# Kernel tuning notes

Measured on AMD Instinct MI355X. Metric: run time of the kernel, lower is better.

## Reference

```python
import jax, jax.numpy as jnp
import numpy as np

N = 20000
E = 320000
IN_FEAT = 256
HID = 256
OUT_FEAT = 128


def setup_inputs() -> dict:
    key = jax.random.key(0)
    ks = jax.random.split(key, 10)
    inp = {
        "x": jax.random.normal(ks[0], (N, IN_FEAT), dtype=jnp.float32),
        "edge_src": jax.random.randint(ks[1], (E,), 0, N, dtype=jnp.int32),
        "edge_dst": jax.random.randint(ks[2], (E,), 0, N, dtype=jnp.int32),
        "edge_w": jax.random.uniform(ks[3], (E,), dtype=jnp.float32),
        # params (Linear weights stored as [out, in], torch convention)
        "W_emb": jax.random.normal(ks[4], (HID, IN_FEAT), dtype=jnp.float32) / np.sqrt(IN_FEAT),
        "W_gc1": jax.random.normal(ks[5], (HID, 2 * HID), dtype=jnp.float32) / np.sqrt(2 * HID),
        "b_gc1": jnp.zeros((HID,), dtype=jnp.float32),
        "W_gc2": jax.random.normal(ks[6], (HID, 2 * HID), dtype=jnp.float32) / np.sqrt(2 * HID),
        "b_gc2": jnp.zeros((HID,), dtype=jnp.float32),
        "W_fc": jax.random.normal(ks[7], (OUT_FEAT, HID), dtype=jnp.float32) / np.sqrt(HID),
    }
    return inp


def reference(x, edge_src, edge_dst, edge_w, W_emb, W_gc1, b_gc1, W_gc2, b_gc2, W_fc):
    n = x.shape[0]

    def adj_mul(h):
        msgs = h[edge_src] * edge_w[:, None]           # [E, hid]
        return jax.ops.segment_sum(msgs, edge_dst, num_segments=n)

    def gconv(h, W, b):
        cat = jnp.concatenate([h, adj_mul(h)], axis=1)  # [N, 2*hid]
        return cat @ W.T + b

    h = x @ W_emb.T                                    # embedding (no bias)
    h = h + jax.nn.relu(gconv(h, W_gc1, b_gc1))        # residual (dropout = eval identity)
    h = h + jax.nn.relu(gconv(h, W_gc2, b_gc2))
    out = h @ W_fc.T                                   # fc_last (no bias)
    out = out / jnp.sqrt(jnp.sum(out * out, axis=1, keepdims=True))
    return out
```

## Files before the change

kernel.cpp:

```cpp
#include <hip/hip_runtime.h>
#include <math.h>

#define N_NODES 20000
#define E_EDGES 320000
#define HID 256
#define OUT_FEAT 128
#define MPAD 20224
#define CAP 64

#define BK 64
#define LSTR 72
#define ISTR 80
#define TSTR 264

typedef __attribute__((ext_vector_type(8))) __bf16 bf16x8;
typedef __attribute__((ext_vector_type(4))) float floatx4;
typedef __attribute__((ext_vector_type(4))) int intx4;

__device__ __forceinline__ void write_int8_shadow(
    const __bf16 (*tile)[TSTR], int row0, int tid,
    unsigned char* __restrict__ h8, float* __restrict__ scl) {
    const int row = tid >> 3;
    const int seg = tid & 7;
    float vals[32];
    float mx = 0.f;
#pragma unroll
    for (int j = 0; j < 32; j++) {
        float v = (float)tile[row][seg * 32 + j];
        vals[j] = v;
        mx = fmaxf(mx, fabsf(v));
    }
#pragma unroll
    for (int m = 1; m <= 4; m <<= 1) mx = fmaxf(mx, __shfl_xor(mx, m));
    const float enc = mx > 0.f ? 127.f / mx : 0.f;
    unsigned int pk[8];
#pragma unroll
    for (int g = 0; g < 8; g++) {
        unsigned int wd = 0;
#pragma unroll
        for (int j = 0; j < 4; j++) {
            int q = (int)rintf(vals[g * 4 + j] * enc);
            q = q > 127 ? 127 : (q < -127 ? -127 : q);
            wd |= ((unsigned int)(q & 0xff)) << (8 * j);
        }
        pk[g] = wd;
    }
    unsigned char* dstp = h8 + (size_t)(row0 + row) * HID + seg * 32;
    *(int4*)dstp        = make_int4(pk[0], pk[1], pk[2], pk[3]);
    *(int4*)(dstp + 16) = make_int4(pk[4], pk[5], pk[6], pk[7]);
    if (seg == 0) scl[row0 + row] = mx * (1.f / 127.f);
}


#define EMB_BLK 316
#define SCAT_BLK 625
#define CONVL_BLK 40
#define CONVR_BLK 64

__global__ __launch_bounds__(512) void front_kernel(
    const float* __restrict__ x, const float* __restrict__ wembf,
    __bf16* __restrict__ hb0, unsigned char* __restrict__ h8, float* __restrict__ scl,
    const int* __restrict__ src, const int* __restrict__ dst,
    const float* __restrict__ w, int* __restrict__ counts, int2* __restrict__ edges,
    const float* __restrict__ w1f, const float* __restrict__ w2f, const float* __restrict__ wfcf,
    __bf16* __restrict__ w1l, __bf16* __restrict__ w2l, __bf16* __restrict__ wfcb,
    unsigned char* __restrict__ w1r8, unsigned char* __restrict__ w2r8,
    float* __restrict__ w1rs, float* __restrict__ w2rs)
{
    __shared__ char smem[64 * 144 + 256 * 144];
    const int bid = blockIdx.x;
    const int tid = threadIdx.x;

    if (bid < EMB_BLK) {
        __bf16* As = (__bf16*)smem;
        __bf16* Bs = (__bf16*)(smem + 64 * 144);
        const int row0 = bid * 64;
        const int wv = tid >> 6, l = tid & 63, lr = l & 15, lq = l >> 4;
        const int wm = wv & 1, wn4 = wv >> 1;

        floatx4 acc[2][4];
#pragma unroll
        for (int i = 0; i < 2; i++)
#pragma unroll
            for (int j = 0; j < 4; j++) acc[i][j] = (floatx4){0.f, 0.f, 0.f, 0.f};

        const int srow = tid >> 3;
        const int skq = (tid & 7) * 8;

        for (int kc = 0; kc < 256; kc += BK) {
            {
                int grow = row0 + srow;
                float4 v0 = make_float4(0.f, 0.f, 0.f, 0.f), v1 = v0;
                if (grow < N_NODES) {
                    const float* xp = x + (size_t)grow * HID + kc + skq;
                    v0 = *(const float4*)xp;
                    v1 = *(const float4*)(xp + 4);
                }
                bf16x8 o;
                o[0] = (__bf16)v0.x; o[1] = (__bf16)v0.y; o[2] = (__bf16)v0.z; o[3] = (__bf16)v0.w;
                o[4] = (__bf16)v1.x; o[5] = (__bf16)v1.y; o[6] = (__bf16)v1.z; o[7] = (__bf16)v1.w;
                *(bf16x8*)&As[srow * LSTR + skq] = o;
            }
#pragma unroll
            for (int r = 0; r < 4; r++) {
                int row = r * 64 + srow;
                const float* wp = wembf + (size_t)row * 256 + kc + skq;
                float4 v0 = *(const float4*)wp;
                float4 v1 = *(const float4*)(wp + 4);
                bf16x8 o;
                o[0] = (__bf16)v0.x; o[1] = (__bf16)v0.y; o[2] = (__bf16)v0.z; o[3] = (__bf16)v0.w;
                o[4] = (__bf16)v1.x; o[5] = (__bf16)v1.y; o[6] = (__bf16)v1.z; o[7] = (__bf16)v1.w;
                *(bf16x8*)&Bs[row * LSTR + skq] = o;
            }
            __syncthreads();
#pragma unroll
            for (int s = 0; s < 2; s++) {
                bf16x8 af[2], bfr[4];
#pragma unroll
                for (int mt = 0; mt < 2; mt++)
                    af[mt] = *(const bf16x8*)&As[(wm * 32 + mt * 16 + lr) * LSTR + s * 32 + lq * 8];
#pragma unroll
                for (int nt = 0; nt < 4; nt++)
                    bfr[nt] = *(const bf16x8*)&Bs[(wn4 * 64 + nt * 16 + lr) * LSTR + s * 32 + lq * 8];
#pragma unroll
                for (int mt = 0; mt < 2; mt++)
#pragma unroll
                    for (int nt = 0; nt < 4; nt++)
                        acc[mt][nt] = __builtin_amdgcn_mfma_f32_16x16x32_bf16(af[mt], bfr[nt], acc[mt][nt], 0, 0, 0);
            }
            __syncthreads();
        }
        __bf16 (*tile)[TSTR] = (__bf16(*)[TSTR])smem;
#pragma unroll
        for (int nt = 0; nt < 4; nt++) {
            const int col = wn4 * 64 + nt * 16 + lr;
#pragma unroll
            for (int mt = 0; mt < 2; mt++) {
                const int lrow = wm * 32 + mt * 16 + lq * 4;
#pragma unroll
                for (int r = 0; r < 4; r++) {
                    float v = acc[mt][nt][r];
                    hb0[(size_t)(row0 + lrow + r) * HID + col] = (__bf16)v;
                    tile[lrow + r][col] = (__bf16)v;
                }
            }
        }
        __syncthreads();
        write_int8_shadow(tile, row0, tid, h8, scl);
    } else if (bid < EMB_BLK + SCAT_BLK) {
        int e = (bid - EMB_BLK) * 512 + tid;
        int d = dst[e];
        int p = atomicAdd(&counts[d], 1);
        edges[(size_t)d * CAP + p] = make_int2(src[e], __float_as_int(w[e]));
    } else if (bid < EMB_BLK + SCAT_BLK + CONVL_BLK) {
        const size_t gi = ((size_t)(bid - EMB_BLK - SCAT_BLK) * 512 + tid) * 8;
        const float* sp; __bf16* dp;
        if (gi < 65536) {
            size_t row = gi >> 8, k = gi & 255;
            sp = w1f + row * 512 + k; dp = w1l + gi;
        } else if (gi < 131072) {
            size_t off = gi - 65536, row = off >> 8, k = off & 255;
            sp = w2f + row * 512 + k; dp = w2l + off;
        } else {
            size_t off = gi - 131072;
            sp = wfcf + off; dp = wfcb + off;
        }
        float4 v0 = *(const float4*)sp;
        float4 v1 = *(const float4*)(sp + 4);
        bf16x8 o;
        o[0] = (__bf16)v0.x; o[1] = (__bf16)v0.y; o[2] = (__bf16)v0.z; o[3] = (__bf16)v0.w;
        o[4] = (__bf16)v1.x; o[5] = (__bf16)v1.y; o[6] = (__bf16)v1.z; o[7] = (__bf16)v1.w;
        *(bf16x8*)dp = o;
    } else {
        const int gw = (bid - EMB_BLK - SCAT_BLK - CONVL_BLK) * 8 + (tid >> 6);
        const int lane = tid & 63;
        const float* Wsrc = (gw < 256) ? w1f : w2f;
        unsigned char* d8 = (gw < 256) ? w1r8 : w2r8;
        float* ds = (gw < 256) ? w1rs : w2rs;
        const int r = gw & 255;
        float4 v = *(const float4*)(Wsrc + (size_t)r * 512 + 256 + lane * 4);
        float mx = fmaxf(fmaxf(fabsf(v.x), fabsf(v.y)), fmaxf(fabsf(v.z), fabsf(v.w)));
#pragma unroll
        for (int m = 1; m <= 32; m <<= 1) mx = fmaxf(mx, __shfl_xor(mx, m));
        const float enc = mx > 0.f ? 127.f / mx : 0.f;
        unsigned int wd = 0;
        float vv[4] = {v.x, v.y, v.z, v.w};
#pragma unroll
        for (int j = 0; j < 4; j++) {
            int q = (int)rintf(vv[j] * enc);
            q = q > 127 ? 127 : (q < -127 ? -127 : q);
            wd |= ((unsigned int)(q & 0xff)) << (8 * j);
        }
        *(unsigned int*)(d8 + (size_t)r * 256 + lane * 4) = wd;
        if (lane == 0) ds[r] = mx * (1.f / 127.f);
    }
}


#define GBM 32
#define AGG_BYTES (4 * GBM * ISTR)
#define ASCL_OFF  AGG_BYTES
#define GEMM_OFF  (AGG_BYTES + 128)
#define TILE_BYTES (GBM * TSTR * 2)

template <bool LAST>
__global__ __launch_bounds__(256, 3) void gconv_kernel(
    const __bf16* __restrict__ hp,
    const unsigned char* __restrict__ h8in, const float* __restrict__ sclin,
    const int* __restrict__ counts, const int2* __restrict__ edges,
    const __bf16* __restrict__ Wl,
    const unsigned char* __restrict__ Wr8, const float* __restrict__ Wrs,
    const float* __restrict__ bias,
    __bf16* __restrict__ hn, unsigned char* __restrict__ h8out, float* __restrict__ sclout,
    const __bf16* __restrict__ Wfc, float* __restrict__ outp)
{
    __shared__ char smem[GEMM_OFF + TILE_BYTES];
    char* As8 = smem;
    float* asclL = (float*)(smem + ASCL_OFF);
    const int tid = threadIdx.x;
    const int row0 = blockIdx.x * GBM;
    const int wv = tid >> 6, l = tid & 63, lr = l & 15, lq = l >> 4;

    {
        const int hw = tid >> 5;
        const int lh = tid & 31;
#pragma unroll 1
        for (int t = 0; t < 4; ++t) {
            const int j = hw * 4 + t;
            const int d = row0 + j;
            const size_t base = (size_t)d * CAP;
            const int cnt = counts[d];
            const int iters = (cnt + 15) >> 4;
            float acc[8];
#pragma unroll
            for (int q = 0; q < 8; q++) acc[q] = 0.f;

            for (int it = 0; it < iters; ++it) {
                const int jb = it * 16;
                const int2* ep = edges + base + jb;
                int4 eh[8];
#pragma unroll
                for (int u = 0; u < 8; u++) eh[u] = *(const int4*)(ep + u * 2);
                int sidx[16]; float ew[16];
#pragma unroll
                for (int u = 0; u < 8; u++) {
                    const bool m0 = (jb + u * 2)     < cnt;
                    const bool m1 = (jb + u * 2 + 1) < cnt;
                    sidx[u * 2]     = m0 ? eh[u].x : 0;
                    ew[u * 2]       = m0 ? __int_as_float(eh[u].y) : 0.f;
                    sidx[u * 2 + 1] = m1 ? eh[u].z : 0;
                    ew[u * 2 + 1]   = m1 ? __int_as_float(eh[u].w) : 0.f;
                }
                float ws[16];
#pragma unroll
                for (int u = 0; u < 16; u++) ws[u] = ew[u] * sclin[sidx[u]];
                uint2 hv[16];
#pragma unroll
                for (int u = 0; u < 16; u++)
                    hv[u] = *(const uint2*)(h8in + (size_t)sidx[u] * HID + lh * 8);
#pragma unroll
                for (int u = 0; u < 16; u++) {
                    const unsigned int a = hv[u].x, b = hv[u].y;
                    const float wu = ws[u];
                    acc[0] = fmaf(wu, (float)(int)(signed char)(a),       acc[0]);
                    acc[1] = fmaf(wu, (float)(int)(signed char)(a >> 8),  acc[1]);
                    acc[2] = fmaf(wu, (float)(int)(signed char)(a >> 16), acc[2]);
                    acc[3] = fmaf(wu, (float)(int)(signed char)(a >> 24), acc[3]);
                    acc[4] = fmaf(wu, (float)(int)(signed char)(b),       acc[4]);
                    acc[5] = fmaf(wu, (float)(int)(signed char)(b >> 8),  acc[5]);
                    acc[6] = fmaf(wu, (float)(int)(signed char)(b >> 16), acc[6]);
                    acc[7] = fmaf(wu, (float)(int)(signed char)(b >> 24), acc[7]);
                }
            }
            float mx = 0.f;
#pragma unroll
            for (int q = 0; q < 8; q++) mx = fmaxf(mx, fabsf(acc[q]));
#pragma unroll
            for (int m = 1; m <= 16; m <<= 1) mx = fmaxf(mx, __shfl_xor(mx, m));
            const float enc = mx > 0.f ? 127.f / mx : 0.f;
            unsigned int w0 = 0, w1v = 0;
#pragma unroll
            for (int jj = 0; jj < 4; jj++) {
                int q0 = (int)rintf(acc[jj] * enc);
                q0 = q0 > 127 ? 127 : (q0 < -127 ? -127 : q0);
                w0 |= ((unsigned int)(q0 & 0xff)) << (8 * jj);
                int q1 = (int)rintf(acc[4 + jj] * enc);
                q1 = q1 > 127 ? 127 : (q1 < -127 ? -127 : q1);
                w1v |= ((unsigned int)(q1 & 0xff)) << (8 * jj);
            }
            *(uint2*)&As8[(((lh >> 3) * GBM) + j) * ISTR + (lh & 7) * 8] = make_uint2(w0, w1v);
            if (lh == 0) asclL[j] = mx * (1.f / 127.f);
        }
    }

    floatx4 acc[2][4];
    intx4 acc8[2][4];
#pragma unroll
    for (int i = 0; i < 2; i++)
#pragma unroll
        for (int j = 0; j < 4; j++) {
            acc[i][j] = (floatx4){0.f, 0.f, 0.f, 0.f};
            acc8[i][j] = (intx4){0, 0, 0, 0};
        }

#pragma unroll
    for (int kc = 0; kc < 256; kc += BK) {
#pragma unroll
        for (int s = 0; s < 2; s++) {
            const int k0 = kc + s * 32 + lq * 8;
            bf16x8 af[2], bfr[4];
#pragma unroll
            for (int mt = 0; mt < 2; mt++)
                af[mt] = *(const bf16x8*)(hp + (size_t)(row0 + mt * 16 + lr) * HID + k0);
#pragma unroll
            for (int nt = 0; nt < 4; nt++)
                bfr[nt] = *(const bf16x8*)(Wl + (size_t)(wv * 64 + nt * 16 + lr) * 256 + k0);
#pragma unroll
            for (int mt = 0; mt < 2; mt++)
#pragma unroll
                for (int nt = 0; nt < 4; nt++)
                    acc[mt][nt] = __builtin_amdgcn_mfma_f32_16x16x32_bf16(af[mt], bfr[nt], acc[mt][nt], 0, 0, 0);
        }
    }

    __syncthreads();

#pragma unroll
    for (int kc = 0; kc < 256; kc += BK) {
        intx4 a8[2], b8[4];
#pragma unroll
        for (int mt = 0; mt < 2; mt++)
            a8[mt] = *(const intx4*)&As8[(((kc >> 6) * GBM) + mt * 16 + lr) * ISTR + lq * 16];
#pragma unroll
        for (int nt = 0; nt < 4; nt++)
            b8[nt] = *(const intx4*)(Wr8 + (size_t)(wv * 64 + nt * 16 + lr) * 256 + kc + lq * 16);
#pragma unroll
        for (int mt = 0; mt < 2; mt++)
#pragma unroll
            for (int nt = 0; nt < 4; nt++)
                acc8[mt][nt] = __builtin_amdgcn_mfma_i32_16x16x64_i8(a8[mt], b8[nt], acc8[mt][nt], 0, 0, 0);
    }

    __bf16 (*tile)[TSTR] = (__bf16(*)[TSTR])(smem + GEMM_OFF);
#pragma unroll
    for (int nt = 0; nt < 4; nt++) {
        const int col = wv * 64 + nt * 16 + lr;
        const float b = bias[col];
        const float wrc = Wrs[col];
#pragma unroll
        for (int mt = 0; mt < 2; mt++) {
            const int lrow = mt * 16 + lq * 4;
#pragma unroll
            for (int r = 0; r < 4; r++) {
                const int row = row0 + lrow + r;
                float gem = acc[mt][nt][r] + (float)acc8[mt][nt][r] * (asclL[lrow + r] * wrc);
                float res = (float)hp[(size_t)row * HID + col];
                float v = res + fmaxf(gem + b, 0.f);
                if (!LAST) hn[(size_t)row * HID + col] = (__bf16)v;
                tile[lrow + r][col] = (__bf16)v;
            }
        }
    }
    __syncthreads();

    if (!LAST) {
        write_int8_shadow(tile, row0, tid, h8out, sclout);
    } else if (wv < 2) {
        floatx4 facc[8];
#pragma unroll
        for (int j = 0; j < 8; j++) facc[j] = (floatx4){0.f, 0.f, 0.f, 0.f};
#pragma unroll
        for (int kt = 0; kt < 256; kt += 32) {
            bf16x8 a = *(const bf16x8*)&tile[wv * 16 + lr][kt + lq * 8];
            bf16x8 bf8[8];
#pragma unroll
            for (int nt = 0; nt < 8; nt++)
                bf8[nt] = *(const bf16x8*)(Wfc + (size_t)(nt * 16 + lr) * 256 + kt + lq * 8);
#pragma unroll
            for (int nt = 0; nt < 8; nt++)
                facc[nt] = __builtin_amdgcn_mfma_f32_16x16x32_bf16(a, bf8[nt], facc[nt], 0, 0, 0);
        }
        float s[4];
#pragma unroll
        for (int r = 0; r < 4; r++) {
            float t = 0.f;
#pragma unroll
            for (int nt = 0; nt < 8; nt++) t = fmaf(facc[nt][r], facc[nt][r], t);
            s[r] = t;
        }
#pragma unroll
        for (int mask = 1; mask <= 8; mask <<= 1) {
#pragma unroll
            for (int r = 0; r < 4; r++) s[r] += __shfl_xor(s[r], mask);
        }
        float inv[4];
#pragma unroll
        for (int r = 0; r < 4; r++) inv[r] = rsqrtf(s[r]);
#pragma unroll
        for (int r = 0; r < 4; r++) {
            int row = row0 + wv * 16 + lq * 4 + r;
            if (row >= N_NODES) continue;
#pragma unroll
            for (int nt = 0; nt < 8; nt++)
                outp[(size_t)row * OUT_FEAT + nt * 16 + lr] = facc[nt][r] * inv[r];
        }
    }
}


extern "C" void kernel_launch(void* const* d_in, const int* in_sizes, int n_in,
                              void* d_out, int out_size, void* d_ws, size_t ws_size,
                              hipStream_t stream) {
    const float* x        = (const float*)d_in[0];
    const int*   edge_src = (const int*)d_in[1];
    const int*   edge_dst = (const int*)d_in[2];
    const float* edge_w   = (const float*)d_in[3];
    const float* W_emb    = (const float*)d_in[4];
    const float* W_gc1    = (const float*)d_in[5];
    const float* b_gc1    = (const float*)d_in[6];
    const float* W_gc2    = (const float*)d_in[7];
    const float* b_gc2    = (const float*)d_in[8];
    const float* W_fc     = (const float*)d_in[9];
    float* out = (float*)d_out;

    char* p = (char*)d_ws;
    const size_t HROW = (size_t)MPAD * HID;
    __bf16* hb0   = (__bf16*)p;             p += HROW * 2;
    __bf16* hb1   = (__bf16*)p;             p += HROW * 2;
    unsigned char* h8a = (unsigned char*)p; p += HROW;
    float*  scla  = (float*)p;              p += (size_t)MPAD * 4;
    unsigned char* h8b = (unsigned char*)p; p += HROW;
    float*  sclb  = (float*)p;              p += (size_t)MPAD * 4;
    __bf16* w1l   = (__bf16*)p;             p += 65536 * 2;
    __bf16* w2l   = (__bf16*)p;             p += 65536 * 2;
    __bf16* wfcb  = (__bf16*)p;             p += 32768 * 2;
    unsigned char* w1r8 = (unsigned char*)p; p += 65536;
    unsigned char* w2r8 = (unsigned char*)p; p += 65536;
    float*  w1rs  = (float*)p;              p += 256 * 4;
    float*  w2rs  = (float*)p;              p += 256 * 4;
    int2*   edges = (int2*)p;               p += (size_t)N_NODES * CAP * 8;
    int*    counts = (int*)p;               p += (size_t)MPAD * 4;

    hipMemsetAsync(counts, 0, (size_t)MPAD * 4, stream);

    front_kernel<<<EMB_BLK + SCAT_BLK + CONVL_BLK + CONVR_BLK, 512, 0, stream>>>(
        x, W_emb, hb0, h8a, scla, edge_src, edge_dst, edge_w, counts, edges,
        W_gc1, W_gc2, W_fc, w1l, w2l, wfcb, w1r8, w2r8, w1rs, w2rs);

    gconv_kernel<false><<<MPAD / GBM, 256, 0, stream>>>(
        hb0, h8a, scla, counts, edges, w1l, w1r8, w1rs, b_gc1,
        hb1, h8b, sclb, nullptr, nullptr);

    gconv_kernel<true><<<MPAD / GBM, 256, 0, stream>>>(
        hb1, h8b, sclb, counts, edges, w2l, w2r8, w2rs, b_gc2,
        nullptr, nullptr, nullptr, wfcb, out);
}
```

Before: 207.6 us.

## Halve gconv row tile and aggregate two rows per wavefront with full-wave lanes

Cuts the gconv block tile from 32 to 16 rows, so the grid has twice as many blocks, and raises the occupancy hint to 4 blocks per CU. Aggregation now maps a full 64-lane wave over the 256-wide feature row (4 bytes per lane) and processes two destination rows at once with interleaved loads, instead of half-waves doing 8 bytes each over 4 rows sequentially. The MFMA GEMMs and epilogue are reduced to a single 16-row M tile, and the int8 shadow writer gains a 16-row variant. Each block now reloads the full weight matrices for half as many rows, which adds weight traffic per output row. Pairing rows also means each pair iterates up to the larger of the two edge counts.

```diff
diff --git a/kernel.cpp b/kernel.cpp
--- a/kernel.cpp
+++ b/kernel.cpp
@@ -17,7 +17,7 @@
 typedef __attribute__((ext_vector_type(4))) float floatx4;
 typedef __attribute__((ext_vector_type(4))) int intx4;
 
-__device__ __forceinline__ void write_int8_shadow(
+__device__ __forceinline__ void write_int8_shadow64(
     const __bf16 (*tile)[TSTR], int row0, int tid,
     unsigned char* __restrict__ h8, float* __restrict__ scl) {
     const int row = tid >> 3;
@@ -48,6 +48,39 @@
     unsigned char* dstp = h8 + (size_t)(row0 + row) * HID + seg * 32;
     *(int4*)dstp        = make_int4(pk[0], pk[1], pk[2], pk[3]);
     *(int4*)(dstp + 16) = make_int4(pk[4], pk[5], pk[6], pk[7]);
+    if (seg == 0) scl[row0 + row] = mx * (1.f / 127.f);
+}
+
+__device__ __forceinline__ void write_int8_shadow16(
+    const __bf16 (*tile)[TSTR], int row0, int tid,
+    unsigned char* __restrict__ h8, float* __restrict__ scl) {
+    const int row = tid >> 4;
+    const int seg = tid & 15;
+    float vals[16];
+    float mx = 0.f;
+#pragma unroll
+    for (int j = 0; j < 16; j++) {
+        float v = (float)tile[row][seg * 16 + j];
+        vals[j] = v;
+        mx = fmaxf(mx, fabsf(v));
+    }
+#pragma unroll
+    for (int m = 1; m <= 8; m <<= 1) mx = fmaxf(mx, __shfl_xor(mx, m));
+    const float enc = mx > 0.f ? 127.f / mx : 0.f;
+    unsigned int pk[4];
+#pragma unroll
+    for (int g = 0; g < 4; g++) {
+        unsigned int wd = 0;
+#pragma unroll
+        for (int j = 0; j < 4; j++) {
+            int q = (int)rintf(vals[g * 4 + j] * enc);
+            q = q > 127 ? 127 : (q < -127 ? -127 : q);
+            wd |= ((unsigned int)(q & 0xff)) << (8 * j);
+        }
+        pk[g] = wd;
+    }
+    unsigned char* dstp = h8 + (size_t)(row0 + row) * HID + seg * 16;
+    *(int4*)dstp = make_int4(pk[0], pk[1], pk[2], pk[3]);
     if (seg == 0) scl[row0 + row] = mx * (1.f / 127.f);
 }
 
@@ -146,7 +179,7 @@
             }
         }
         __syncthreads();
-        write_int8_shadow(tile, row0, tid, h8, scl);
+        write_int8_shadow64(tile, row0, tid, h8, scl);
     } else if (bid < EMB_BLK + SCAT_BLK) {
         int e = (bid - EMB_BLK) * 512 + tid;
         int d = dst[e];
@@ -197,14 +230,14 @@
 }
 
 
-#define GBM 32
+#define GBM 16
 #define AGG_BYTES (4 * GBM * ISTR)
 #define ASCL_OFF  AGG_BYTES
 #define GEMM_OFF  (AGG_BYTES + 128)
 #define TILE_BYTES (GBM * TSTR * 2)
 
 template <bool LAST>
-__global__ __launch_bounds__(256, 3) void gconv_kernel(
+__global__ __launch_bounds__(256, 4) void gconv_kernel(
     const __bf16* __restrict__ hp,
     const unsigned char* __restrict__ h8in, const float* __restrict__ sclin,
     const int* __restrict__ counts, const int2* __restrict__ edges,
@@ -222,104 +255,124 @@
     const int wv = tid >> 6, l = tid & 63, lr = l & 15, lq = l >> 4;
 
     {
-        const int hw = tid >> 5;
-        const int lh = tid & 31;
+        const int w4 = wv * 4;
+        int cnts[4];
+#pragma unroll
+        for (int k = 0; k < 4; k++) cnts[k] = counts[row0 + w4 + k];
 #pragma unroll 1
-        for (int t = 0; t < 4; ++t) {
-            const int j = hw * 4 + t;
-            const int d = row0 + j;
-            const size_t base = (size_t)d * CAP;
-            const int cnt = counts[d];
-            const int iters = (cnt + 15) >> 4;
-            float acc[8];
-#pragma unroll
-            for (int q = 0; q < 8; q++) acc[q] = 0.f;
-
-            for (int it = 0; it < iters; ++it) {
+        for (int pp = 0; pp < 2; ++pp) {
+            const int jA = w4 + pp * 2, jB = jA + 1;
+            const int cntA = cnts[pp * 2], cntB = cnts[pp * 2 + 1];
+            const int cm = cntA > cntB ? cntA : cntB;
+            const int itm = (cm + 15) >> 4;
+            const int2* epA = edges + (size_t)(row0 + jA) * CAP;
+            const int2* epB = edges + (size_t)(row0 + jB) * CAP;
+            float accA[4] = {0.f, 0.f, 0.f, 0.f};
+            float accB[4] = {0.f, 0.f, 0.f, 0.f};
+#pragma unroll 1
+            for (int it = 0; it < itm; ++it) {
                 const int jb = it * 16;
-                const int2* ep = edges + base + jb;
-                int4 eh[8];
-#pragma unroll
-                for (int u = 0; u < 8; u++) eh[u] = *(const int4*)(ep + u * 2);
-                int sidx[16]; float ew[16];
+                int4 ehA[8], ehB[8];
+#pragma unroll
+                for (int u = 0; u < 8; u++) ehA[u] = *(const int4*)(epA + jb + u * 2);
+#pragma unroll
+                for (int u = 0; u < 8; u++) ehB[u] = *(const int4*)(epB + jb + u * 2);
+                float wsA[16]; unsigned int hA[16];
 #pragma unroll
                 for (int u = 0; u < 8; u++) {
-                    const bool m0 = (jb + u * 2)     < cnt;
-                    const bool m1 = (jb + u * 2 + 1) < cnt;
-                    sidx[u * 2]     = m0 ? eh[u].x : 0;
-                    ew[u * 2]       = m0 ? __int_as_float(eh[u].y) : 0.f;
-                    sidx[u * 2 + 1] = m1 ? eh[u].z : 0;
-                    ew[u * 2 + 1]   = m1 ? __int_as_float(eh[u].w) : 0.f;
+                    const bool m0 = (jb + u * 2)     < cntA;
+                    const bool m1 = (jb + u * 2 + 1) < cntA;
+                    const int s0 = m0 ? ehA[u].x : 0;
+                    const int s1 = m1 ? ehA[u].z : 0;
+                    const float w0 = m0 ? __int_as_float(ehA[u].y) : 0.f;
+                    const float w1 = m1 ? __int_as_float(ehA[u].w) : 0.f;
+                    wsA[u * 2]     = w0 * sclin[s0];
+                    wsA[u * 2 + 1] = w1 * sclin[s1];
+                    hA[u * 2]     = *(const unsigned int*)(h8in + (size_t)s0 * HID + l * 4);
+                    hA[u * 2 + 1] = *(const unsigned int*)(h8in + (size_t)s1 * HID + l * 4);
                 }
-                float ws[16];
-#pragma unroll
-                for (int u = 0; u < 16; u++) ws[u] = ew[u] * sclin[sidx[u]];
-                uint2 hv[16];
-#pragma unroll
-                for (int u = 0; u < 16; u++)
-                    hv[u] = *(const uint2*)(h8in + (size_t)sidx[u] * HID + lh * 8);
+                float wsB[16]; unsigned int hB[16];
+#pragma unroll
+                for (int u = 0; u < 8; u++) {
+                    const bool m0 = (jb + u * 2)     < cntB;
+                    const bool m1 = (jb + u * 2 + 1) < cntB;
+                    const int s0 = m0 ? ehB[u].x : 0;
+                    const int s1 = m1 ? ehB[u].z : 0;
+                    const float w0 = m0 ? __int_as_float(ehB[u].y) : 0.f;
+                    const float w1 = m1 ? __int_as_float(ehB[u].w) : 0.f;
+                    wsB[u * 2]     = w0 * sclin[s0];
+                    wsB[u * 2 + 1] = w1 * sclin[s1];
+                    hB[u * 2]     = *(const unsigned int*)(h8in + (size_t)s0 * HID + l * 4);
+                    hB[u * 2 + 1] = *(const unsigned int*)(h8in + (size_t)s1 * HID + l * 4);
+                }
 #pragma unroll
                 for (int u = 0; u < 16; u++) {
-                    const unsigned int a = hv[u].x, b = hv[u].y;
-                    const float wu = ws[u];
-                    acc[0] = fmaf(wu, (float)(int)(signed char)(a),       acc[0]);
-                    acc[1] = fmaf(wu, (float)(int)(signed char)(a >> 8),  acc[1]);
-                    acc[2] = fmaf(wu, (float)(int)(signed char)(a >> 16), acc[2]);
-                    acc[3] = fmaf(wu, (float)(int)(signed char)(a >> 24), acc[3]);
-                    acc[4] = fmaf(wu, (float)(int)(signed char)(b),       acc[4]);
-                    acc[5] = fmaf(wu, (float)(int)(signed char)(b >> 8),  acc[5]);
-                    acc[6] = fmaf(wu, (float)(int)(signed char)(b >> 16), acc[6]);
-                    acc[7] = fmaf(wu, (float)(int)(signed char)(b >> 24), acc[7]);
+                    const unsigned int a = hA[u];
+                    const float w = wsA[u];
+                    accA[0] = fmaf(w, (float)(int)(signed char)(a),       accA[0]);
+                    accA[1] = fmaf(w, (float)(int)(signed char)(a >> 8),  accA[1]);
+                    accA[2] = fmaf(w, (float)(int)(signed char)(a >> 16), accA[2]);
+                    accA[3] = fmaf(w, (float)(int)(signed char)(a >> 24), accA[3]);
                 }
-            }
-            float mx = 0.f;
-#pragma unroll
-            for (int q = 0; q < 8; q++) mx = fmaxf(mx, fabsf(acc[q]));
-#pragma unroll
-            for (int m = 1; m <= 16; m <<= 1) mx = fmaxf(mx, __shfl_xor(mx, m));
-            const float enc = mx > 0.f ? 127.f / mx : 0.f;
-            unsigned int w0 = 0, w1v = 0;
-#pragma unroll
-            for (int jj = 0; jj < 4; jj++) {
-                int q0 = (int)rintf(acc[jj] * enc);
-                q0 = q0 > 127 ? 127 : (q0 < -127 ? -127 : q0);
-                w0 |= ((unsigned int)(q0 & 0xff)) << (8 * jj);
-                int q1 = (int)rintf(acc[4 + jj] * enc);
-                q1 = q1 > 127 ? 127 : (q1 < -127 ? -127 : q1);
-                w1v |= ((unsigned int)(q1 & 0xff)) << (8 * jj);
-            }
-            *(uint2*)&As8[(((lh >> 3) * GBM) + j) * ISTR + (lh & 7) * 8] = make_uint2(w0, w1v);
-            if (lh == 0) asclL[j] = mx * (1.f / 127.f);
-        }
-    }
-
-    floatx4 acc[2][4];
-    intx4 acc8[2][4];
-#pragma unroll
-    for (int i = 0; i < 2; i++)
-#pragma unroll
-        for (int j = 0; j < 4; j++) {
-            acc[i][j] = (floatx4){0.f, 0.f, 0.f, 0.f};
-            acc8[i][j] = (intx4){0, 0, 0, 0};
-        }
+#pragma unroll
+                for (int u = 0; u < 16; u++) {
+                    const unsigned int a = hB[u];
+                    const float w = wsB[u];
+                    accB[0] = fmaf(w, (float)(int)(signed char)(a),       accB[0]);
+                    accB[1] = fmaf(w, (float)(int)(signed char)(a >> 8),  accB[1]);
+                    accB[2] = fmaf(w, (float)(int)(signed char)(a >> 16), accB[2]);
+                    accB[3] = fmaf(w, (float)(int)(signed char)(a >> 24), accB[3]);
+                }
+            }
+            float mA = fmaxf(fmaxf(fabsf(accA[0]), fabsf(accA[1])), fmaxf(fabsf(accA[2]), fabsf(accA[3])));
+            float mB = fmaxf(fmaxf(fabsf(accB[0]), fabsf(accB[1])), fmaxf(fabsf(accB[2]), fabsf(accB[3])));
+#pragma unroll
+            for (int m = 1; m <= 32; m <<= 1) {
+                mA = fmaxf(mA, __shfl_xor(mA, m));
+                mB = fmaxf(mB, __shfl_xor(mB, m));
+            }
+            const float encA = mA > 0.f ? 127.f / mA : 0.f;
+            const float encB = mB > 0.f ? 127.f / mB : 0.f;
+            unsigned int wdA = 0, wdB = 0;
+#pragma unroll
+            for (int j = 0; j < 4; j++) {
+                int qa = (int)rintf(accA[j] * encA);
+                qa = qa > 127 ? 127 : (qa < -127 ? -127 : qa);
+                wdA |= ((unsigned int)(qa & 0xff)) << (8 * j);
+                int qb = (int)rintf(accB[j] * encB);
+                qb = qb > 127 ? 127 : (qb < -127 ? -127 : qb);
+                wdB |= ((unsigned int)(qb & 0xff)) << (8 * j);
+            }
+            *(unsigned int*)&As8[(((l >> 4) * GBM) + jA) * ISTR + (l & 15) * 4] = wdA;
+            *(unsigned int*)&As8[(((l >> 4) * GBM) + jB) * ISTR + (l & 15) * 4] = wdB;
+            if (l == 0) {
+                asclL[jA] = mA * (1.f / 127.f);
+                asclL[jB] = mB * (1.f / 127.f);
+            }
+        }
+    }
+
+    floatx4 acc[4];
+    intx4 acc8[4];
+#pragma unroll
+    for (int j = 0; j < 4; j++) {
+        acc[j] = (floatx4){0.f, 0.f, 0.f, 0.f};
+        acc8[j] = (intx4){0, 0, 0, 0};
+    }
 
 #pragma unroll
     for (int kc = 0; kc < 256; kc += BK) {
 #pragma unroll
         for (int s = 0; s < 2; s++) {
             const int k0 = kc + s * 32 + lq * 8;
-            bf16x8 af[2], bfr[4];
-#pragma unroll
-            for (int mt = 0; mt < 2; mt++)
-                af[mt] = *(const bf16x8*)(hp + (size_t)(row0 + mt * 16 + lr) * HID + k0);
+            bf16x8 af = *(const bf16x8*)(hp + (size_t)(row0 + lr) * HID + k0);
+            bf16x8 bfr[4];
 #pragma unroll
             for (int nt = 0; nt < 4; nt++)
                 bfr[nt] = *(const bf16x8*)(Wl + (size_t)(wv * 64 + nt * 16 + lr) * 256 + k0);
 #pragma unroll
-            for (int mt = 0; mt < 2; mt++)
-#pragma unroll
-                for (int nt = 0; nt < 4; nt++)
-                    acc[mt][nt] = __builtin_amdgcn_mfma_f32_16x16x32_bf16(af[mt], bfr[nt], acc[mt][nt], 0, 0, 0);
+            for (int nt = 0; nt < 4; nt++)
+                acc[nt] = __builtin_amdgcn_mfma_f32_16x16x32_bf16(af, bfr[nt], acc[nt], 0, 0, 0);
         }
     }
 
@@ -327,18 +380,14 @@
 
 #pragma unroll
     for (int kc = 0; kc < 256; kc += BK) {
-        intx4 a8[2], b8[4];
-#pragma unroll
-        for (int mt = 0; mt < 2; mt++)
-            a8[mt] = *(const intx4*)&As8[(((kc >> 6) * GBM) + mt * 16 + lr) * ISTR + lq * 16];
+        intx4 a8 = *(const intx4*)&As8[(((kc >> 6) * GBM) + lr) * ISTR + lq * 16];
+        intx4 b8[4];
 #pragma unroll
         for (int nt = 0; nt < 4; nt++)
             b8[nt] = *(const intx4*)(Wr8 + (size_t)(wv * 64 + nt * 16 + lr) * 256 + kc + lq * 16);
 #pragma unroll
-        for (int mt = 0; mt < 2; mt++)
-#pragma unroll
-            for (int nt = 0; nt < 4; nt++)
-                acc8[mt][nt] = __builtin_amdgcn_mfma_i32_16x16x64_i8(a8[mt], b8[nt], acc8[mt][nt], 0, 0, 0);
+        for (int nt = 0; nt < 4; nt++)
+            acc8[nt] = __builtin_amdgcn_mfma_i32_16x16x64_i8(a8, b8[nt], acc8[nt], 0, 0, 0);
     }
 
     __bf16 (*tile)[TSTR] = (__bf16(*)[TSTR])(smem + GEMM_OFF);
@@ -348,30 +397,27 @@
         const float b = bias[col];
         const float wrc = Wrs[col];
 #pragma unroll
-        for (int mt = 0; mt < 2; mt++) {
-            const int lrow = mt * 16 + lq * 4;
-#pragma unroll
-            for (int r = 0; r < 4; r++) {
-                const int row = row0 + lrow + r;
-                float gem = acc[mt][nt][r] + (float)acc8[mt][nt][r] * (asclL[lrow + r] * wrc);
-                float res = (float)hp[(size_t)row * HID + col];
-                float v = res + fmaxf(gem + b, 0.f);
-                if (!LAST) hn[(size_t)row * HID + col] = (__bf16)v;
-                tile[lrow + r][col] = (__bf16)v;
-            }
+        for (int r = 0; r < 4; r++) {
+            const int lrow = lq * 4 + r;
+            const int row = row0 + lrow;
+            float gem = acc[nt][r] + (float)acc8[nt][r] * (asclL[lrow] * wrc);
+            float res = (float)hp[(size_t)row * HID + col];
+            float v = res + fmaxf(gem + b, 0.f);
+            if (!LAST) hn[(size_t)row * HID + col] = (__bf16)v;
+            tile[lrow][col] = (__bf16)v;
         }
     }
     __syncthreads();
 
     if (!LAST) {
-        write_int8_shadow(tile, row0, tid, h8out, sclout);
-    } else if (wv < 2) {
+        write_int8_shadow16(tile, row0, tid, h8out, sclout);
+    } else if (wv == 0) {
         floatx4 facc[8];
 #pragma unroll
         for (int j = 0; j < 8; j++) facc[j] = (floatx4){0.f, 0.f, 0.f, 0.f};
 #pragma unroll
         for (int kt = 0; kt < 256; kt += 32) {
-            bf16x8 a = *(const bf16x8*)&tile[wv * 16 + lr][kt + lq * 8];
+            bf16x8 a = *(const bf16x8*)&tile[lr][kt + lq * 8];
             bf16x8 bf8[8];
 #pragma unroll
             for (int nt = 0; nt < 8; nt++)
@@ -398,7 +444,7 @@
         for (int r = 0; r < 4; r++) inv[r] = rsqrtf(s[r]);
 #pragma unroll
         for (int r = 0; r < 4; r++) {
-            int row = row0 + wv * 16 + lq * 4 + r;
+            int row = row0 + lq * 4 + r;
             if (row >= N_NODES) continue;
 #pragma unroll
             for (int nt = 0; nt < 8; nt++)
```

Result: slower. 279.3 us (+34.5%).
